# Performance work log

Hardware: AMD Instinct MI355X
Metric: run time of the kernel (lower is better)

## Reference

```python
import jax, jax.numpy as jnp
import numpy as np

B, SQ, SKV, D, H = 2, 2048, 2048, 1024, 16
DH = D // H


def setup_inputs() -> dict:
    key = jax.random.key(0)
    ks = jax.random.split(key, 4)
    s = 0.02
    return {
        "query_input": jax.random.normal(ks[0], (B, SQ, D), jnp.float32),
        "kv_input": jax.random.normal(ks[1], (B, SKV, D), jnp.float32),
        "Wq": jax.random.normal(ks[2], (D, D), jnp.float32) * s,
        "bq": jnp.zeros((D,), jnp.float32),
        "Wkv": jax.random.normal(ks[3], (D, 2 * D), jnp.float32) * s,
        "bkv": jnp.zeros((2 * D,), jnp.float32),
        "Wo": jax.random.normal(jax.random.fold_in(key, 7), (D, D), jnp.float32) * s,
        "bo": jnp.zeros((D,), jnp.float32),
    }


def reference(query_input, kv_input, Wq, bq, Wkv, bkv, Wo, bo):
    scale = 1.0 / jnp.sqrt(jnp.float32(DH))
    # Projections
    q = query_input @ Wq + bq                      # [B, SQ, D]
    kv = kv_input @ Wkv + bkv                      # [B, SKV, 2D]
    k, v = jnp.split(kv, 2, axis=-1)               # [B, SKV, D] each
    # Split heads: [B, H, S, DH]
    q = q.reshape(B, SQ, H, DH).transpose(0, 2, 1, 3)
    k = k.reshape(B, SKV, H, DH).transpose(0, 2, 1, 3)
    v = v.reshape(B, SKV, H, DH).transpose(0, 2, 1, 3)
    # Scores S = QK^T / sqrt(d_k)
    scores = jnp.einsum("bhqd,bhkd->bhqk", q, k) * scale
    attn = jax.nn.softmax(scores, axis=-1)
    out = jnp.einsum("bhqk,bhkd->bhqd", attn, v)   # [B, H, SQ, DH]
    out = out.transpose(0, 2, 1, 3).reshape(B, SQ, D)
    return out @ Wo + bo
```

## Files before the change

kernel.cpp:

```cpp
#include <hip/hip_runtime.h>

typedef unsigned short u16;
typedef unsigned int u32;
typedef __bf16 bf16x8 __attribute__((ext_vector_type(8)));
typedef float f32x4 __attribute__((ext_vector_type(4)));

#define QSCALE 0.18033688011112f

__device__ __forceinline__ u16 f2bf(float f) {
  u32 u = __builtin_bit_cast(u32, f);
  u += 0x7fffu + ((u >> 16) & 1u);
  return (u16)(u >> 16);
}

__device__ __forceinline__ bf16x8 as_bf16x8(uint4 v) {
  return __builtin_bit_cast(bf16x8, v);
}

__device__ __forceinline__ void async16(const void* g, void* l) {
  __builtin_amdgcn_global_load_lds(
      (__attribute__((address_space(1))) void*)(g),
      (__attribute__((address_space(3))) void*)(l), 16, 0, 0);
}

__global__ void prep_kernel(const float* __restrict__ xq, const float* __restrict__ xkv,
                            const float* __restrict__ Wq, const float* __restrict__ Wkv,
                            const float* __restrict__ Wo,
                            u16* __restrict__ Xq16, u16* __restrict__ Xkv16,
                            u16* __restrict__ WqT, u16* __restrict__ WkvT,
                            u16* __restrict__ WoT) {
  const int bid = blockIdx.x, tid = threadIdx.x;
  if (bid < 8192) {
    int i = bid * 256 + tid;
    const float* s; u16* d; int j;
    if (i < 1048576) { s = xq; d = Xq16; j = i; }
    else             { s = xkv; d = Xkv16; j = i - 1048576; }
    float4 v = ((const float4*)s)[j];
    ushort4 o;
    o.x = f2bf(v.x); o.y = f2bf(v.y); o.z = f2bf(v.z); o.w = f2bf(v.w);
    ((ushort4*)d)[j] = o;
    return;
  }
  const int b2 = bid - 8192;
  const int z = b2 >> 11, rem = b2 & 2047;
  const int by = rem >> 6, bx = rem & 63;
  const float* src; u16* dst; int Nd;
  if (z == 0)      { src = Wq;  dst = WqT;  Nd = 1024; }
  else if (z == 1) { src = Wkv; dst = WkvT; Nd = 2048; }
  else             { src = Wo;  dst = WoT;  Nd = 1024; }
  const int n0 = bx * 32, k0 = by * 32;
  if (n0 >= Nd) return;
  __shared__ float tile[32][33];
  const int tx = tid & 31, ty = tid >> 5;
#pragma unroll
  for (int j = 0; j < 4; ++j)
    tile[ty + 8 * j][tx] = src[(size_t)(k0 + ty + 8 * j) * Nd + n0 + tx];
  __syncthreads();
#pragma unroll
  for (int j = 0; j < 4; ++j)
    dst[(size_t)(n0 + ty + 8 * j) * 1024 + k0 + tx] = f2bf(tile[tx][ty + 8 * j]);
}

template <int MI>
static __device__ __forceinline__ void gemm_core(
    const u16* __restrict__ A, const u16* __restrict__ Bt, int m0,
    uint4* sA, uint4* sB, f32x4 (*acc)[4]) {
  const int tid = threadIdx.x;
  const int wv = tid >> 6, lane = tid & 63;
  const int quad = lane >> 4, l16 = lane & 15;
  const int wm = (wv >> 1) * (MI * 16), wn = (wv & 1) * 64;

  const int ib0 = wv * 128 + lane, ib1 = ib0 + 64;
  const int br0 = ib0 >> 2, bc0 = (ib0 & 3) ^ ((br0 >> 1) & 3);
  const int br1 = ib1 >> 2, bc1 = (ib1 & 3) ^ ((br1 >> 1) & 3);
  const u16* gB0 = Bt + (size_t)br0 * 1024 + bc0 * 8;
  const u16* gB1 = Bt + (size_t)br1 * 1024 + bc1 * 8;

  const int ia0 = wv * (MI * 32) + lane;
  const int ar0 = ia0 >> 2, ac0 = (ia0 & 3) ^ ((ar0 >> 1) & 3);
  const u16* gA0 = A + (size_t)(m0 + ar0) * 1024 + ac0 * 8;
  const int ia1 = ia0 + 64;
  const int ar1 = ia1 >> 2, ac1 = (ia1 & 3) ^ ((ar1 >> 1) & 3);
  const u16* gA1 = A + (size_t)(m0 + ar1) * 1024 + ac1 * 8;
  uint4* sAw = sA + wv * (MI * 32);
  uint4* sBw = sB + wv * 128;

  for (int k0 = 0; k0 < 1024; k0 += 32) {
    __syncthreads();
    async16(gA0 + k0, sAw);
    if (MI == 4) async16(gA1 + k0, sAw + 64);
    async16(gB0 + k0, sBw);
    async16(gB1 + k0, sBw + 64);
    __syncthreads();

    bf16x8 af[MI], bfr[4];
#pragma unroll
    for (int mi = 0; mi < MI; ++mi) {
      int r = wm + mi * 16 + l16;
      af[mi] = as_bf16x8(sA[r * 4 + (quad ^ ((r >> 1) & 3))]);
    }
#pragma unroll
    for (int ni = 0; ni < 4; ++ni) {
      int r = wn + ni * 16 + l16;
      bfr[ni] = as_bf16x8(sB[r * 4 + (quad ^ ((r >> 1) & 3))]);
    }
#pragma unroll
    for (int mi = 0; mi < MI; ++mi)
#pragma unroll
      for (int ni = 0; ni < 4; ++ni)
        acc[mi][ni] = __builtin_amdgcn_mfma_f32_16x16x32_bf16(
            af[mi], bfr[ni], acc[mi][ni], 0, 0, 0);
  }
}

__global__ __launch_bounds__(256, 2) void gemm_qkv(
    const u16* __restrict__ Xq, const u16* __restrict__ Xkv,
    const u16* __restrict__ WqT, const u16* __restrict__ WkvT,
    const float* __restrict__ bq, const float* __restrict__ bkv,
    u16* __restrict__ Qd, u16* __restrict__ Kd, u16* __restrict__ Vd) {
  __shared__ uint4 sA[512], sB[512];
  f32x4 acc[4][4] = {};
  const int n0 = blockIdx.x * 128, m0 = blockIdx.y * 128;
  const u16* A = (n0 < 1024) ? Xq : Xkv;
  const u16* Bt = (n0 < 1024) ? (WqT + (size_t)n0 * 1024)
                              : (WkvT + (size_t)(n0 - 1024) * 1024);
  const float* bias = (n0 < 1024) ? (bq + n0) : (bkv + (n0 - 1024));
  gemm_core<4>(A, Bt, m0, sA, sB, acc);

  const int tid = threadIdx.x, wv = tid >> 6, lane = tid & 63;
  const int quad = lane >> 4, l16 = lane & 15;
  const int wm = (wv >> 1) * 64, wn = (wv & 1) * 64;
  const int bb = m0 >> 11;
  const int ssb = (m0 & 2047) + wm + quad * 4;
#pragma unroll
  for (int ni = 0; ni < 4; ++ni) {
    const int gn = n0 + wn + ni * 16 + l16;
    const float bvn = bias[wn + ni * 16 + l16];
    if (gn < 2048) {
      u16* dst = (gn < 1024) ? Qd : Kd;
      const float sc = (gn < 1024) ? QSCALE : 1.0f;
      const int col = gn & 1023, hh = col >> 6, dh = col & 63;
      u16* base = dst + (size_t)(bb * 16 + hh) * 2048 * 64 + dh;
#pragma unroll
      for (int mi = 0; mi < 4; ++mi)
#pragma unroll
        for (int r = 0; r < 4; ++r)
          base[(size_t)(ssb + mi * 16 + r) * 64] = f2bf((acc[mi][ni][r] + bvn) * sc);
    } else {
      const int col = gn - 2048, hh = col >> 6, dh = col & 63;
      u16* base = Vd + ((size_t)(bb * 16 + hh) * 64 + dh) * 2048;
#pragma unroll
      for (int mi = 0; mi < 4; ++mi)
#pragma unroll
        for (int r = 0; r < 4; ++r)
          base[ssb + mi * 16 + r] = f2bf(acc[mi][ni][r] + bvn);
    }
  }
}

__global__ __launch_bounds__(256, 2) void flash_attn(
    const u16* __restrict__ Q, const u16* __restrict__ K,
    const u16* __restrict__ V, u16* __restrict__ O) {
  __shared__ uint4 sK[2][512];
  __shared__ uint4 sV[2][512];
  __shared__ __align__(16) u16 sP[4][32][72];

  const int tid = threadIdx.x;
  const int wv = tid >> 6, lane = tid & 63;
  const int quad = lane >> 4, l16 = lane & 15;
  const int q0 = blockIdx.x * 128;
  const size_t bh = blockIdx.z * 16 + blockIdx.y;

  const u16* Qb = Q + (bh * 2048 + q0) * 64;
  const u16* Kb = K + bh * 2048 * 64;
  const u16* Vb = V + bh * 64 * 2048;

  bf16x8 qf[2][2];
#pragma unroll
  for (int rb = 0; rb < 2; ++rb) {
    const uint4* qp = (const uint4*)(Qb + (size_t)(wv * 32 + rb * 16 + l16) * 64);
    qf[rb][0] = as_bf16x8(qp[quad]);
    qf[rb][1] = as_bf16x8(qp[4 + quad]);
  }

  f32x4 oacc[2][4] = {};
  f32x4 lsum[2] = {};
  const uint4 ones4 = {0x3F803F80u, 0x3F803F80u, 0x3F803F80u, 0x3F803F80u};
  const bf16x8 ones = as_bf16x8(ones4);

  const int i0 = wv * 128 + lane, i1 = i0 + 64;
  const int kr0 = i0 >> 3, kr1 = i1 >> 3;
  const int kck0 = (i0 & 7) ^ ((i0 >> 5) & 7);
  const int kck1 = (i1 & 7) ^ ((i1 >> 5) & 7);
  const int vck0 = (i0 & 7) ^ (kr0 & 7);
  const int vck1 = (i1 & 7) ^ (kr1 & 7);
  const u16* gK0 = Kb + (size_t)kr0 * 64 + kck0 * 8;
  const u16* gK1 = Kb + (size_t)kr1 * 64 + kck1 * 8;
  const u16* gV0 = Vb + (size_t)kr0 * 2048 + vck0 * 8;
  const u16* gV1 = Vb + (size_t)kr1 * 2048 + vck1 * 8;
  const int wo = wv * 128;

  async16(gK0, &sK[0][wo]);
  async16(gK1, &sK[0][wo + 64]);
  async16(gV0, &sV[0][wo]);
  async16(gV1, &sV[0][wo + 64]);

  for (int t = 0; t < 32; ++t) {
    const int cur = t & 1;
    __syncthreads();
    if (t < 31) {
      const int nxt = cur ^ 1;
      const size_t ko = (size_t)(t + 1) * 4096;
      const int vo = (t + 1) * 64;
      async16(gK0 + ko, &sK[nxt][wo]);
      async16(gK1 + ko, &sK[nxt][wo + 64]);
      async16(gV0 + vo, &sV[nxt][wo]);
      async16(gV1 + vo, &sV[nxt][wo + 64]);
    }
    const uint4* K_ = sK[cur];
    const uint4* V_ = sV[cur];

    bf16x8 bK0[4], bK1[4];
#pragma unroll
    for (int ni = 0; ni < 4; ++ni) {
      int rr = l16 * 4 + ni;
      bK0[ni] = as_bf16x8(K_[rr * 8 + (quad ^ (l16 & 7))]);
      bK1[ni] = as_bf16x8(K_[rr * 8 + ((4 + quad) ^ (l16 & 7))]);
    }

#pragma unroll
    for (int rb = 0; rb < 2; ++rb) {
      f32x4 s4[4];
#pragma unroll
      for (int ni = 0; ni < 4; ++ni) {
        f32x4 a = {0.f, 0.f, 0.f, 0.f};
        a = __builtin_amdgcn_mfma_f32_16x16x32_bf16(qf[rb][0], bK0[ni], a, 0, 0, 0);
        a = __builtin_amdgcn_mfma_f32_16x16x32_bf16(qf[rb][1], bK1[ni], a, 0, 0, 0);
        s4[ni] = a;
      }
#pragma unroll
      for (int r = 0; r < 4; ++r) {
        u32 u0 = __builtin_bit_cast(u32, exp2f(s4[0][r])) + 0x8000u;
        u32 u1 = __builtin_bit_cast(u32, exp2f(s4[1][r])) + 0x8000u;
        u32 u2 = __builtin_bit_cast(u32, exp2f(s4[2][r])) + 0x8000u;
        u32 u3 = __builtin_bit_cast(u32, exp2f(s4[3][r])) + 0x8000u;
        uint2 pk;
        pk.x = (u0 >> 16) | (u1 & 0xFFFF0000u);
        pk.y = (u2 >> 16) | (u3 & 0xFFFF0000u);
        *(uint2*)&sP[wv][rb * 16 + quad * 4 + r][l16 * 4] = pk;
      }
    }

    bf16x8 vf0[4], vf1[4];
#pragma unroll
    for (int ni = 0; ni < 4; ++ni) {
      int rr = ni * 16 + l16;
      vf0[ni] = as_bf16x8(V_[rr * 8 + (quad ^ (rr & 7))]);
      vf1[ni] = as_bf16x8(V_[rr * 8 + ((4 + quad) ^ (rr & 7))]);
    }
#pragma unroll
    for (int rb = 0; rb < 2; ++rb) {
      bf16x8 pf0 = as_bf16x8(*(const uint4*)&sP[wv][rb * 16 + l16][quad * 8]);
      bf16x8 pf1 = as_bf16x8(*(const uint4*)&sP[wv][rb * 16 + l16][32 + quad * 8]);
      lsum[rb] = __builtin_amdgcn_mfma_f32_16x16x32_bf16(pf0, ones, lsum[rb], 0, 0, 0);
      lsum[rb] = __builtin_amdgcn_mfma_f32_16x16x32_bf16(pf1, ones, lsum[rb], 0, 0, 0);
#pragma unroll
      for (int ni = 0; ni < 4; ++ni) {
        oacc[rb][ni] = __builtin_amdgcn_mfma_f32_16x16x32_bf16(pf0, vf0[ni], oacc[rb][ni], 0, 0, 0);
        oacc[rb][ni] = __builtin_amdgcn_mfma_f32_16x16x32_bf16(pf1, vf1[ni], oacc[rb][ni], 0, 0, 0);
      }
    }
  }

#pragma unroll
  for (int rb = 0; rb < 2; ++rb) {
    u16* Ob = O + ((size_t)(blockIdx.z * 2048 + q0 + wv * 32 + rb * 16 + quad * 4)) * 1024
                + blockIdx.y * 64;
#pragma unroll
    for (int r = 0; r < 4; ++r) {
      float rl = 1.0f / lsum[rb][r];
#pragma unroll
      for (int ni = 0; ni < 4; ++ni)
        Ob[(size_t)r * 1024 + ni * 16 + l16] = f2bf(oacc[rb][ni][r] * rl);
    }
  }
}

__global__ __launch_bounds__(256, 2) void gemm_out(
    const u16* __restrict__ A, const u16* __restrict__ Bt,
    const float* __restrict__ bias, float* __restrict__ C) {
  __shared__ uint4 sA[256], sB[512];
  f32x4 acc[2][4] = {};
  const int n0 = blockIdx.x * 128, m0 = blockIdx.y * 64;
  gemm_core<2>(A, Bt + (size_t)n0 * 1024, m0, sA, sB, acc);

  const int tid = threadIdx.x, wv = tid >> 6, lane = tid & 63;
  const int quad = lane >> 4, l16 = lane & 15;
  const int wm = (wv >> 1) * 32, wn = (wv & 1) * 64;
  float bv[4];
#pragma unroll
  for (int ni = 0; ni < 4; ++ni) bv[ni] = bias[n0 + wn + ni * 16 + l16];
#pragma unroll
  for (int mi = 0; mi < 2; ++mi)
#pragma unroll
    for (int ni = 0; ni < 4; ++ni)
#pragma unroll
      for (int r = 0; r < 4; ++r) {
        int gm = m0 + wm + mi * 16 + quad * 4 + r;
        int gn = n0 + wn + ni * 16 + l16;
        C[(size_t)gm * 1024 + gn] = acc[mi][ni][r] + bv[ni];
      }
}

extern "C" void kernel_launch(void* const* d_in, const int* in_sizes, int n_in,
                              void* d_out, int out_size, void* d_ws, size_t ws_size,
                              hipStream_t stream) {
  const float* xq  = (const float*)d_in[0];
  const float* xkv = (const float*)d_in[1];
  const float* Wq  = (const float*)d_in[2];
  const float* bq  = (const float*)d_in[3];
  const float* Wkv = (const float*)d_in[4];
  const float* bkv = (const float*)d_in[5];
  const float* Wo  = (const float*)d_in[6];
  const float* bo  = (const float*)d_in[7];
  float* out = (float*)d_out;

  char* p = (char*)d_ws;
  u16* Xq16  = (u16*)p; p += (size_t)8 << 20;
  u16* Xkv16 = (u16*)p; p += (size_t)8 << 20;
  u16* WqT   = (u16*)p; p += (size_t)2 << 20;
  u16* WkvT  = (u16*)p; p += (size_t)4 << 20;
  u16* WoT   = (u16*)p; p += (size_t)2 << 20;
  u16* Q16   = (u16*)p; p += (size_t)8 << 20;
  u16* K16   = (u16*)p; p += (size_t)8 << 20;
  u16* Vt16  = (u16*)p; p += (size_t)8 << 20;
  u16* O16   = (u16*)p; p += (size_t)8 << 20;

  prep_kernel<<<14336, 256, 0, stream>>>(xq, xkv, Wq, Wkv, Wo,
                                         Xq16, Xkv16, WqT, WkvT, WoT);
  gemm_qkv<<<dim3(24, 32), 256, 0, stream>>>(Xq16, Xkv16, WqT, WkvT, bq, bkv,
                                             Q16, K16, Vt16);
  flash_attn<<<dim3(16, 16, 2), 256, 0, stream>>>(Q16, K16, Vt16, O16);
  gemm_out<<<dim3(8, 64), 256, 0, stream>>>(O16, WoT, bo, out);
}
```

Before: 224.7 us.

## Store Q/K row-major, vectorize V stores, shrink attention blocks to two waves

The QKV GEMM epilogue now writes Q and K in plain [B,S,D] row-major layout instead of a per-head layout, and packs V^T stores into ushort4 writes. The flash attention kernel reads Q/K with stride 1024, uses 128-thread blocks over 64 query rows with twice as many blocks, and replaces the double-buffered async K/V prefetch with a single buffer loaded and synced every tile. This is meant to make the epilogue writes cheaper and raise occupancy, at the cost of losing load/compute overlap in attention and adding a second barrier per tile.

```diff
diff --git a/kernel.cpp b/kernel.cpp
--- a/kernel.cpp
+++ b/kernel.cpp
@@ -131,54 +131,63 @@
   const int quad = lane >> 4, l16 = lane & 15;
   const int wm = (wv >> 1) * 64, wn = (wv & 1) * 64;
   const int bb = m0 >> 11;
+  const int gmb = m0 + wm + quad * 4;
   const int ssb = (m0 & 2047) + wm + quad * 4;
 #pragma unroll
   for (int ni = 0; ni < 4; ++ni) {
     const int gn = n0 + wn + ni * 16 + l16;
     const float bvn = bias[wn + ni * 16 + l16];
-    if (gn < 2048) {
-      u16* dst = (gn < 1024) ? Qd : Kd;
-      const float sc = (gn < 1024) ? QSCALE : 1.0f;
-      const int col = gn & 1023, hh = col >> 6, dh = col & 63;
-      u16* base = dst + (size_t)(bb * 16 + hh) * 2048 * 64 + dh;
+    if (gn < 1024) {
+      u16* base = Qd + gn;
 #pragma unroll
       for (int mi = 0; mi < 4; ++mi)
 #pragma unroll
         for (int r = 0; r < 4; ++r)
-          base[(size_t)(ssb + mi * 16 + r) * 64] = f2bf((acc[mi][ni][r] + bvn) * sc);
+          base[(size_t)(gmb + mi * 16 + r) * 1024] = f2bf((acc[mi][ni][r] + bvn) * QSCALE);
+    } else if (gn < 2048) {
+      u16* base = Kd + (gn - 1024);
+#pragma unroll
+      for (int mi = 0; mi < 4; ++mi)
+#pragma unroll
+        for (int r = 0; r < 4; ++r)
+          base[(size_t)(gmb + mi * 16 + r) * 1024] = f2bf(acc[mi][ni][r] + bvn);
     } else {
       const int col = gn - 2048, hh = col >> 6, dh = col & 63;
-      u16* base = Vd + ((size_t)(bb * 16 + hh) * 64 + dh) * 2048;
-#pragma unroll
-      for (int mi = 0; mi < 4; ++mi)
-#pragma unroll
-        for (int r = 0; r < 4; ++r)
-          base[ssb + mi * 16 + r] = f2bf(acc[mi][ni][r] + bvn);
-    }
-  }
-}
-
-__global__ __launch_bounds__(256, 2) void flash_attn(
+      u16* base = Vd + ((size_t)(bb * 16 + hh) * 64 + dh) * 2048 + ssb;
+#pragma unroll
+      for (int mi = 0; mi < 4; ++mi) {
+        ushort4 o;
+        o.x = f2bf(acc[mi][ni][0] + bvn);
+        o.y = f2bf(acc[mi][ni][1] + bvn);
+        o.z = f2bf(acc[mi][ni][2] + bvn);
+        o.w = f2bf(acc[mi][ni][3] + bvn);
+        *(ushort4*)(base + mi * 16) = o;
+      }
+    }
+  }
+}
+
+__global__ __launch_bounds__(128, 3) void flash_attn(
     const u16* __restrict__ Q, const u16* __restrict__ K,
     const u16* __restrict__ V, u16* __restrict__ O) {
-  __shared__ uint4 sK[2][512];
-  __shared__ uint4 sV[2][512];
-  __shared__ __align__(16) u16 sP[4][32][72];
+  __shared__ uint4 sK[512];
+  __shared__ uint4 sV[512];
+  __shared__ __align__(16) u16 sP[2][32][72];
 
   const int tid = threadIdx.x;
   const int wv = tid >> 6, lane = tid & 63;
   const int quad = lane >> 4, l16 = lane & 15;
-  const int q0 = blockIdx.x * 128;
-  const size_t bh = blockIdx.z * 16 + blockIdx.y;
-
-  const u16* Qb = Q + (bh * 2048 + q0) * 64;
-  const u16* Kb = K + bh * 2048 * 64;
-  const u16* Vb = V + bh * 64 * 2048;
+  const int q0 = blockIdx.x * 64;
+  const int h = blockIdx.y;
+
+  const u16* Qb = Q + ((size_t)(blockIdx.z * 2048 + q0)) * 1024 + h * 64;
+  const u16* Kb = K + ((size_t)(blockIdx.z * 2048)) * 1024 + h * 64;
+  const u16* Vb = V + ((size_t)(blockIdx.z * 16 + h)) * 64 * 2048;
 
   bf16x8 qf[2][2];
 #pragma unroll
   for (int rb = 0; rb < 2; ++rb) {
-    const uint4* qp = (const uint4*)(Qb + (size_t)(wv * 32 + rb * 16 + l16) * 64);
+    const uint4* qp = (const uint4*)(Qb + (size_t)(wv * 32 + rb * 16 + l16) * 1024);
     qf[rb][0] = as_bf16x8(qp[quad]);
     qf[rb][1] = as_bf16x8(qp[4 + quad]);
   }
@@ -188,44 +197,35 @@
   const uint4 ones4 = {0x3F803F80u, 0x3F803F80u, 0x3F803F80u, 0x3F803F80u};
   const bf16x8 ones = as_bf16x8(ones4);
 
-  const int i0 = wv * 128 + lane, i1 = i0 + 64;
-  const int kr0 = i0 >> 3, kr1 = i1 >> 3;
-  const int kck0 = (i0 & 7) ^ ((i0 >> 5) & 7);
-  const int kck1 = (i1 & 7) ^ ((i1 >> 5) & 7);
-  const int vck0 = (i0 & 7) ^ (kr0 & 7);
-  const int vck1 = (i1 & 7) ^ (kr1 & 7);
-  const u16* gK0 = Kb + (size_t)kr0 * 64 + kck0 * 8;
-  const u16* gK1 = Kb + (size_t)kr1 * 64 + kck1 * 8;
-  const u16* gV0 = Vb + (size_t)kr0 * 2048 + vck0 * 8;
-  const u16* gV1 = Vb + (size_t)kr1 * 2048 + vck1 * 8;
-  const int wo = wv * 128;
-
-  async16(gK0, &sK[0][wo]);
-  async16(gK1, &sK[0][wo + 64]);
-  async16(gV0, &sV[0][wo]);
-  async16(gV1, &sV[0][wo + 64]);
+  const u16* gK[4]; const u16* gV[4];
+#pragma unroll
+  for (int j = 0; j < 4; ++j) {
+    int i = wv * 256 + j * 64 + lane;
+    int r = i >> 3;
+    int ck = (i & 7) ^ ((r >> 2) & 7);
+    int cv = (i & 7) ^ (r & 7);
+    gK[j] = Kb + (size_t)r * 1024 + ck * 8;
+    gV[j] = Vb + (size_t)r * 2048 + cv * 8;
+  }
+  uint4* sKw = sK + wv * 256;
+  uint4* sVw = sV + wv * 256;
 
   for (int t = 0; t < 32; ++t) {
-    const int cur = t & 1;
+    const int skv0 = t * 64;
     __syncthreads();
-    if (t < 31) {
-      const int nxt = cur ^ 1;
-      const size_t ko = (size_t)(t + 1) * 4096;
-      const int vo = (t + 1) * 64;
-      async16(gK0 + ko, &sK[nxt][wo]);
-      async16(gK1 + ko, &sK[nxt][wo + 64]);
-      async16(gV0 + vo, &sV[nxt][wo]);
-      async16(gV1 + vo, &sV[nxt][wo + 64]);
-    }
-    const uint4* K_ = sK[cur];
-    const uint4* V_ = sV[cur];
+#pragma unroll
+    for (int j = 0; j < 4; ++j) {
+      async16(gK[j] + (size_t)skv0 * 1024, sKw + j * 64);
+      async16(gV[j] + skv0, sVw + j * 64);
+    }
+    __syncthreads();
 
     bf16x8 bK0[4], bK1[4];
 #pragma unroll
     for (int ni = 0; ni < 4; ++ni) {
       int rr = l16 * 4 + ni;
-      bK0[ni] = as_bf16x8(K_[rr * 8 + (quad ^ (l16 & 7))]);
-      bK1[ni] = as_bf16x8(K_[rr * 8 + ((4 + quad) ^ (l16 & 7))]);
+      bK0[ni] = as_bf16x8(sK[rr * 8 + (quad ^ (l16 & 7))]);
+      bK1[ni] = as_bf16x8(sK[rr * 8 + ((4 + quad) ^ (l16 & 7))]);
     }
 
 #pragma unroll
@@ -255,8 +255,8 @@
 #pragma unroll
     for (int ni = 0; ni < 4; ++ni) {
       int rr = ni * 16 + l16;
-      vf0[ni] = as_bf16x8(V_[rr * 8 + (quad ^ (rr & 7))]);
-      vf1[ni] = as_bf16x8(V_[rr * 8 + ((4 + quad) ^ (rr & 7))]);
+      vf0[ni] = as_bf16x8(sV[rr * 8 + (quad ^ (rr & 7))]);
+      vf1[ni] = as_bf16x8(sV[rr * 8 + ((4 + quad) ^ (rr & 7))]);
     }
 #pragma unroll
     for (int rb = 0; rb < 2; ++rb) {
@@ -275,7 +275,7 @@
 #pragma unroll
   for (int rb = 0; rb < 2; ++rb) {
     u16* Ob = O + ((size_t)(blockIdx.z * 2048 + q0 + wv * 32 + rb * 16 + quad * 4)) * 1024
-                + blockIdx.y * 64;
+                + h * 64;
 #pragma unroll
     for (int r = 0; r < 4; ++r) {
       float rl = 1.0f / lsum[rb][r];
@@ -340,6 +340,6 @@
                                          Xq16, Xkv16, WqT, WkvT, WoT);
   gemm_qkv<<<dim3(24, 32), 256, 0, stream>>>(Xq16, Xkv16, WqT, WkvT, bq, bkv,
                                              Q16, K16, Vt16);
-  flash_attn<<<dim3(16, 16, 2), 256, 0, stream>>>(Q16, K16, Vt16, O16);
+  flash_attn<<<dim3(32, 16, 2), 128, 0, stream>>>(Q16, K16, Vt16, O16);
   gemm_out<<<dim3(8, 64), 256, 0, stream>>>(O16, WoT, bo, out);
 }
```

New measurement: 235.0 us. 4.6% more time.

## Split attention over KV halves with atomic fp32 accumulation and combine pass

Applied to the files above, without the earlier changes.

The flash attention grid doubles by splitting the 2048-long KV range into two halves per block. Each half adds its unnormalised output and row sums into fp32 buffers with atomics, and a new combine kernel normalises the result and converts it to bf16. Q and K are now written row-major (token x 1024) instead of head-major, V stores are vectorised to ushort4, and occupancy for flash_attn is raised to 3 blocks per SM. The split relies on the kernel not subtracting a running max, so partial sums add directly. It costs extra memsets, fp32 atomic traffic and one more launch.

```diff
diff --git a/kernel.cpp b/kernel.cpp
--- a/kernel.cpp
+++ b/kernel.cpp
@@ -131,36 +131,46 @@
   const int quad = lane >> 4, l16 = lane & 15;
   const int wm = (wv >> 1) * 64, wn = (wv & 1) * 64;
   const int bb = m0 >> 11;
+  const int gmb = m0 + wm + quad * 4;
   const int ssb = (m0 & 2047) + wm + quad * 4;
 #pragma unroll
   for (int ni = 0; ni < 4; ++ni) {
     const int gn = n0 + wn + ni * 16 + l16;
     const float bvn = bias[wn + ni * 16 + l16];
-    if (gn < 2048) {
-      u16* dst = (gn < 1024) ? Qd : Kd;
-      const float sc = (gn < 1024) ? QSCALE : 1.0f;
-      const int col = gn & 1023, hh = col >> 6, dh = col & 63;
-      u16* base = dst + (size_t)(bb * 16 + hh) * 2048 * 64 + dh;
+    if (gn < 1024) {
+      u16* base = Qd + gn;
 #pragma unroll
       for (int mi = 0; mi < 4; ++mi)
 #pragma unroll
         for (int r = 0; r < 4; ++r)
-          base[(size_t)(ssb + mi * 16 + r) * 64] = f2bf((acc[mi][ni][r] + bvn) * sc);
+          base[(size_t)(gmb + mi * 16 + r) * 1024] = f2bf((acc[mi][ni][r] + bvn) * QSCALE);
+    } else if (gn < 2048) {
+      u16* base = Kd + (gn - 1024);
+#pragma unroll
+      for (int mi = 0; mi < 4; ++mi)
+#pragma unroll
+        for (int r = 0; r < 4; ++r)
+          base[(size_t)(gmb + mi * 16 + r) * 1024] = f2bf(acc[mi][ni][r] + bvn);
     } else {
       const int col = gn - 2048, hh = col >> 6, dh = col & 63;
-      u16* base = Vd + ((size_t)(bb * 16 + hh) * 64 + dh) * 2048;
-#pragma unroll
-      for (int mi = 0; mi < 4; ++mi)
-#pragma unroll
-        for (int r = 0; r < 4; ++r)
-          base[ssb + mi * 16 + r] = f2bf(acc[mi][ni][r] + bvn);
-    }
-  }
-}
-
-__global__ __launch_bounds__(256, 2) void flash_attn(
+      u16* base = Vd + ((size_t)(bb * 16 + hh) * 64 + dh) * 2048 + ssb;
+#pragma unroll
+      for (int mi = 0; mi < 4; ++mi) {
+        ushort4 o;
+        o.x = f2bf(acc[mi][ni][0] + bvn);
+        o.y = f2bf(acc[mi][ni][1] + bvn);
+        o.z = f2bf(acc[mi][ni][2] + bvn);
+        o.w = f2bf(acc[mi][ni][3] + bvn);
+        *(ushort4*)(base + mi * 16) = o;
+      }
+    }
+  }
+}
+
+__global__ __launch_bounds__(256, 3) void flash_attn(
     const u16* __restrict__ Q, const u16* __restrict__ K,
-    const u16* __restrict__ V, u16* __restrict__ O) {
+    const u16* __restrict__ V, float* __restrict__ Onum,
+    float* __restrict__ Lsum) {
   __shared__ uint4 sK[2][512];
   __shared__ uint4 sV[2][512];
   __shared__ __align__(16) u16 sP[4][32][72];
@@ -169,16 +179,18 @@
   const int wv = tid >> 6, lane = tid & 63;
   const int quad = lane >> 4, l16 = lane & 15;
   const int q0 = blockIdx.x * 128;
-  const size_t bh = blockIdx.z * 16 + blockIdx.y;
-
-  const u16* Qb = Q + (bh * 2048 + q0) * 64;
-  const u16* Kb = K + bh * 2048 * 64;
-  const u16* Vb = V + bh * 64 * 2048;
+  const int h = blockIdx.y;
+  const int bz = blockIdx.z >> 1, split = blockIdx.z & 1;
+  const int kv0 = split * 1024;
+
+  const u16* Qb = Q + ((size_t)(bz * 2048 + q0)) * 1024 + h * 64;
+  const u16* Kb = K + ((size_t)(bz * 2048 + kv0)) * 1024 + h * 64;
+  const u16* Vb = V + ((size_t)(bz * 16 + h)) * 64 * 2048 + kv0;
 
   bf16x8 qf[2][2];
 #pragma unroll
   for (int rb = 0; rb < 2; ++rb) {
-    const uint4* qp = (const uint4*)(Qb + (size_t)(wv * 32 + rb * 16 + l16) * 64);
+    const uint4* qp = (const uint4*)(Qb + (size_t)(wv * 32 + rb * 16 + l16) * 1024);
     qf[rb][0] = as_bf16x8(qp[quad]);
     qf[rb][1] = as_bf16x8(qp[4 + quad]);
   }
@@ -194,8 +206,8 @@
   const int kck1 = (i1 & 7) ^ ((i1 >> 5) & 7);
   const int vck0 = (i0 & 7) ^ (kr0 & 7);
   const int vck1 = (i1 & 7) ^ (kr1 & 7);
-  const u16* gK0 = Kb + (size_t)kr0 * 64 + kck0 * 8;
-  const u16* gK1 = Kb + (size_t)kr1 * 64 + kck1 * 8;
+  const u16* gK0 = Kb + (size_t)kr0 * 1024 + kck0 * 8;
+  const u16* gK1 = Kb + (size_t)kr1 * 1024 + kck1 * 8;
   const u16* gV0 = Vb + (size_t)kr0 * 2048 + vck0 * 8;
   const u16* gV1 = Vb + (size_t)kr1 * 2048 + vck1 * 8;
   const int wo = wv * 128;
@@ -205,12 +217,12 @@
   async16(gV0, &sV[0][wo]);
   async16(gV1, &sV[0][wo + 64]);
 
-  for (int t = 0; t < 32; ++t) {
+  for (int t = 0; t < 16; ++t) {
     const int cur = t & 1;
     __syncthreads();
-    if (t < 31) {
+    if (t < 15) {
       const int nxt = cur ^ 1;
-      const size_t ko = (size_t)(t + 1) * 4096;
+      const size_t ko = (size_t)(t + 1) * 64 * 1024;
       const int vo = (t + 1) * 64;
       async16(gK0 + ko, &sK[nxt][wo]);
       async16(gK1 + ko, &sK[nxt][wo + 64]);
@@ -274,16 +286,30 @@
 
 #pragma unroll
   for (int rb = 0; rb < 2; ++rb) {
-    u16* Ob = O + ((size_t)(blockIdx.z * 2048 + q0 + wv * 32 + rb * 16 + quad * 4)) * 1024
-                + blockIdx.y * 64;
-#pragma unroll
-    for (int r = 0; r < 4; ++r) {
-      float rl = 1.0f / lsum[rb][r];
+    const int row = bz * 2048 + q0 + wv * 32 + rb * 16 + quad * 4;
+    float* On = Onum + (size_t)row * 1024 + h * 64;
+#pragma unroll
+    for (int r = 0; r < 4; ++r)
 #pragma unroll
       for (int ni = 0; ni < 4; ++ni)
-        Ob[(size_t)r * 1024 + ni * 16 + l16] = f2bf(oacc[rb][ni][r] * rl);
-    }
-  }
+        atomicAdd(&On[(size_t)r * 1024 + ni * 16 + l16], oacc[rb][ni][r]);
+    if (l16 == 0)
+#pragma unroll
+      for (int r = 0; r < 4; ++r)
+        atomicAdd(&Lsum[(size_t)(row + r) * 16 + h], lsum[rb][r]);
+  }
+}
+
+__global__ void combine_kernel(const float* __restrict__ Onum,
+                               const float* __restrict__ Lsum,
+                               u16* __restrict__ O16) {
+  const int row = blockIdx.x, t = threadIdx.x;
+  const float rl = 1.0f / Lsum[(size_t)row * 16 + (t >> 4)];
+  float4 v = ((const float4*)(Onum + (size_t)row * 1024))[t];
+  ushort4 o;
+  o.x = f2bf(v.x * rl); o.y = f2bf(v.y * rl);
+  o.z = f2bf(v.z * rl); o.w = f2bf(v.w * rl);
+  ((ushort4*)(O16 + (size_t)row * 1024))[t] = o;
 }
 
 __global__ __launch_bounds__(256, 2) void gemm_out(
@@ -335,11 +361,16 @@
   u16* K16   = (u16*)p; p += (size_t)8 << 20;
   u16* Vt16  = (u16*)p; p += (size_t)8 << 20;
   u16* O16   = (u16*)p; p += (size_t)8 << 20;
+  float* Lsum = (float*)p; p += (size_t)256 << 10;
+  float* Onum = (float*)Xq16;
 
   prep_kernel<<<14336, 256, 0, stream>>>(xq, xkv, Wq, Wkv, Wo,
                                          Xq16, Xkv16, WqT, WkvT, WoT);
   gemm_qkv<<<dim3(24, 32), 256, 0, stream>>>(Xq16, Xkv16, WqT, WkvT, bq, bkv,
                                              Q16, K16, Vt16);
-  flash_attn<<<dim3(16, 16, 2), 256, 0, stream>>>(Q16, K16, Vt16, O16);
+  hipMemsetAsync(Onum, 0, (size_t)16 << 20, stream);
+  hipMemsetAsync(Lsum, 0, (size_t)256 << 10, stream);
+  flash_attn<<<dim3(16, 16, 4), 256, 0, stream>>>(Q16, K16, Vt16, Onum, Lsum);
+  combine_kernel<<<4096, 256, 0, stream>>>(Onum, Lsum, O16);
   gemm_out<<<dim3(8, 64), 256, 0, stream>>>(O16, WoT, bo, out);
 }
```

New measurement: 251.6 us. 11.9% more time.
